# Optimization experiments

Hardware: AMD Instinct MI355X
Metric: run time of the kernel (lower is better)

Reference implementation:

```python
import jax, jax.numpy as jnp
import numpy as np

EPS = 1e-6   # torch pairwise_distance eps added inside the norm
MARGIN = 1.0


def setup_inputs() -> dict:
    key = jax.random.key(0)
    k1, k2 = jax.random.split(key)
    B, K, D = 4096, 1024, 128
    input_features = jax.random.normal(k1, (B, D), dtype=jnp.float32)
    centroids = jax.random.normal(k2, (K, D), dtype=jnp.float32)
    return {"input_features": input_features, "centroids": centroids}


def _mode_rows(idx, num_classes):
    # idx: [B, D] ints in [0, num_classes). Returns per-row mode [B].
    # torch.mode returns the smallest value among ties; jnp.argmax also
    # returns the first (smallest) index among ties, so behavior matches.
    B = idx.shape[0]
    counts = jnp.zeros((B, num_classes), jnp.int32)
    counts = counts.at[jnp.arange(B)[:, None], idx].add(1)
    return jnp.argmax(counts, axis=1)


def reference(input_features, centroids):
    B, D = input_features.shape
    K = centroids.shape[0]

    # [B, K, D] per-dimension squared differences (mse_loss with reduce=False)
    sq = (input_features[:, None, :] - centroids[None, :, :]) ** 2
    idx_min = jnp.argmin(sq, axis=1)  # [B, D] closest centroid per dim
    idx_max = jnp.argmax(sq, axis=1)  # [B, D] furthest centroid per dim

    positives = centroids[_mode_rows(idx_min, K)]  # [B, D]
    negatives = centroids[_mode_rows(idx_max, K)]  # [B, D]

    # triplet_margin_loss(margin=1, p=2, swap=True, reduction='mean');
    # torch adds eps inside the norm: ||a - b + eps||_2
    d_pos = jnp.linalg.norm(input_features - positives + EPS, axis=1)
    d_neg = jnp.linalg.norm(input_features - negatives + EPS, axis=1)
    d_swap = jnp.linalg.norm(positives - negatives + EPS, axis=1)
    d_neg = jnp.minimum(d_neg, d_swap)

    return jnp.mean(jnp.maximum(d_pos - d_neg + MARGIN, 0.0))
```

## Files before the change

### kernel.cpp

```cpp
#include <hip/hip_runtime.h>
#include <cstdint>

#define D 128
#define K 1024
#define NB 4096
#define BB 8
#define TK 64
#define FEPS 1e-6f

typedef unsigned long long u64;
typedef unsigned int u32;
typedef unsigned short u16;


__device__ __forceinline__ int vbin(float v, float vmin, float scale) {
    float fb = (v - vmin) * scale;
    fb = fminf(fmaxf(fb, 0.0f), 255.0f);
    return (int)fb;
}

__global__ __launch_bounds__(512) void prep_search_kernel(
    const float* __restrict__ cen, const float* __restrict__ x,
    u16* __restrict__ iminT, float* __restrict__ ext, float* __restrict__ out)
{
    __shared__ u64 bkeys[K];
    __shared__ u64 skeys[K];
    __shared__ float svs[K];
    __shared__ u16 shs[K];
    __shared__ u32 binstart[257];
    __shared__ u32 pfx[256];
    __shared__ u32 cursor[256];
    __shared__ float redmn[8], redmx[8];

    const int dcol = blockIdx.x;
    const int t = threadIdx.x;
    const int wave = t >> 6, lane = t & 63;
    if (dcol == 0 && t == 0) out[0] = 0.0f;

    const float v0 = cen[t * D + dcol];
    const float v1 = cen[(t + 512) * D + dcol];

    float mn = fminf(v0, v1), mx = fmaxf(v0, v1);
    #pragma unroll
    for (int s = 32; s >= 1; s >>= 1) {
        mn = fminf(mn, __shfl_xor(mn, s, 64));
        mx = fmaxf(mx, __shfl_xor(mx, s, 64));
    }
    if (lane == 0) { redmn[wave] = mn; redmx[wave] = mx; }
    if (t < 257) binstart[t] = 0u;
    if (t < 256) cursor[t] = 0u;
    __syncthreads();

    float vmin = redmn[0], vmax = redmx[0];
    #pragma unroll
    for (int w = 1; w < 8; ++w) {
        vmin = fminf(vmin, redmn[w]);
        vmax = fmaxf(vmax, redmx[w]);
    }
    const float range = vmax - vmin;
    const float scale = (range > 0.0f) ? (255.0f / range) : 0.0f;

    u32 u0 = __float_as_uint(v0), u1 = __float_as_uint(v1);
    u0 = (u0 & 0x80000000u) ? ~u0 : (u0 | 0x80000000u);
    u1 = (u1 & 0x80000000u) ? ~u1 : (u1 | 0x80000000u);
    const u64 k0 = ((u64)u0 << 32) | (u32)t;
    const u64 k1 = ((u64)u1 << 32) | (u32)(t + 512);
    const int b0v = vbin(v0, vmin, scale);
    const int b1v = vbin(v1, vmin, scale);
    atomicAdd(&binstart[b0v], 1u);
    atomicAdd(&binstart[b1v], 1u);
    __syncthreads();

    u32 myh = 0u;
    if (t < 256) { myh = binstart[t]; pfx[t] = myh; }
    __syncthreads();
    #pragma unroll
    for (int s = 1; s < 256; s <<= 1) {
        u32 add = 0u;
        if (t < 256 && t >= s) add = pfx[t - s];
        __syncthreads();
        if (t < 256) pfx[t] += add;
        __syncthreads();
    }
    if (t < 256) {
        u32 st = pfx[t] - myh;
        binstart[t] = st;
        cursor[t] = st;
    }
    if (t == 0) binstart[256] = K;
    __syncthreads();

    { u32 s0 = atomicAdd(&cursor[b0v], 1u); bkeys[s0] = k0; }
    { u32 s1 = atomicAdd(&cursor[b1v], 1u); bkeys[s1] = k1; }
    __syncthreads();

    {
        int lo = (int)binstart[b0v], hi = (int)binstart[b0v + 1];
        int r = lo;
        for (int p = lo; p < hi; ++p) r += (bkeys[p] < k0) ? 1 : 0;
        skeys[r] = k0;
    }
    {
        int lo = (int)binstart[b1v], hi = (int)binstart[b1v + 1];
        int r = lo;
        for (int p = lo; p < hi; ++p) r += (bkeys[p] < k1) ? 1 : 0;
        skeys[r] = k1;
    }
    __syncthreads();

    #pragma unroll
    for (int j = 0; j < 2; ++j) {
        int p = j * 512 + t;
        u64 kp = skeys[p];
        u32 vb = (u32)(kp >> 32);
        int p0 = p;
        while (p0 > 0 && (u32)(skeys[p0 - 1] >> 32) == vb) --p0;
        int head = (int)(skeys[p0] & 1023u);
        u32 u = (vb & 0x80000000u) ? (vb & 0x7FFFFFFFu) : ~vb;
        float v = __uint_as_float(u);
        svs[p] = v;
        shs[p] = (u16)head;
        if (p == 0)     { ext[dcol]     = v; ((int*)ext)[2 * D + dcol] = head; }
        if (p == K - 1) { ext[D + dcol] = v; ((int*)ext)[3 * D + dcol] = head; }
    }
    __syncthreads();

    #pragma unroll 1
    for (int ph = 0; ph < 2; ++ph) {
        const int b0 = ph * 2048;
        float xq[4];
        #pragma unroll
        for (int j = 0; j < 4; ++j)
            xq[j] = x[(size_t)(b0 + j * 512 + t) * D + dcol];

        #pragma unroll
        for (int r = 0; r < 4; ++r) {
            const float xv = xq[r];
            const int bx = vbin(xv, vmin, scale);
            int lo = (int)binstart[bx], hi = (int)binstart[bx + 1];
            while (lo < hi) {
                int mid = (lo + hi) >> 1;
                if (svs[mid] <= xv) lo = mid + 1; else hi = mid;
            }
            const int p1 = lo - 1, p2 = lo;
            const int c1 = p1 < 0 ? 0 : p1;
            const int c2 = p2 > K - 1 ? K - 1 : p2;
            float vv1 = svs[c1], vv2 = svs[c2];
            int h1 = shs[c1], h2 = shs[c2];
            float d1 = xv - vv1, d2 = xv - vv2;
            float s1 = d1 * d1, s2 = d2 * d2;
            if (p1 < 0) s1 = 3.4e38f;
            if (p2 > K - 1) s2 = 3.4e38f;
            int idx;
            if (s1 < s2) idx = h1;
            else if (s2 < s1) idx = h2;
            else idx = h1 < h2 ? h1 : h2;
            iminT[(size_t)dcol * NB + b0 + r * 512 + t] = (u16)idx;
        }
    }
}

__global__ __launch_bounds__(256) void mode_loss_kernel(
    const float* __restrict__ x, const float* __restrict__ cen,
    const u16* __restrict__ iminT, const float* __restrict__ ext,
    float* __restrict__ out)
{
    __shared__ float xs[BB * D];
    __shared__ u32 cntA[BB * K / 4];
    __shared__ u32 cntB[BB * K / 4];
    __shared__ int modes[2 * BB];

    const int t = threadIdx.x;
    const int b0 = blockIdx.x * BB;

    ((float4*)xs)[t] = ((const float4*)(x + (size_t)b0 * D))[t];
    {
        uint4 z = make_uint4(0u, 0u, 0u, 0u);
        uint4* a4 = (uint4*)cntA;
        uint4* b4 = (uint4*)cntB;
        #pragma unroll
        for (int j = 0; j < 2; ++j) { a4[t + 256 * j] = z; b4[t + 256 * j] = z; }
    }
    __syncthreads();

    {
        const int dd = t >> 1, half = t & 1;
        uint2 w = *(const uint2*)(iminT + (size_t)dd * NB + b0 + half * 4);
        int i0 = (int)(w.x & 0xFFFFu), i1 = (int)(w.x >> 16);
        int i2 = (int)(w.y & 0xFFFFu), i3 = (int)(w.y >> 16);
        const int rr = half * 4;
        atomicAdd(&cntA[((rr + 0) << 8) + (i0 >> 2)], 1u << ((i0 & 3) * 8));
        atomicAdd(&cntA[((rr + 1) << 8) + (i1 >> 2)], 1u << ((i1 & 3) * 8));
        atomicAdd(&cntA[((rr + 2) << 8) + (i2 >> 2)], 1u << ((i2 & 3) * 8));
        atomicAdd(&cntA[((rr + 3) << 8) + (i3 >> 2)], 1u << ((i3 & 3) * 8));
    }

    const int d = t & (D - 1);
    const int g = t >> 7;
    {
        float cminv = ext[d], cmaxv = ext[D + d];
        int cmini = ((const int*)ext)[2 * D + d];
        int cmaxi = ((const int*)ext)[3 * D + d];
        #pragma unroll
        for (int r = 0; r < 4; ++r) {
            float xv = xs[(g * 4 + r) * D + d];
            float d1 = xv - cminv;
            float d2 = xv - cmaxv;
            float s1 = d1 * d1, s2 = d2 * d2;
            int idx;
            if (s1 > s2) idx = cmini;
            else if (s2 > s1) idx = cmaxi;
            else idx = (cmini < cmaxi) ? cmini : cmaxi;
            const int rr = g * 4 + r;
            atomicAdd(&cntB[(rr << 8) + (idx >> 2)], 1u << ((idx & 3) * 8));
        }
    }
    __syncthreads();

    const int row = t >> 5;
    const int lane = t & 31;
    {
        u32 bkeyA = 0u, bkeyB = 0u;
        #pragma unroll
        for (int j = 0; j < 8; ++j) {
            const int w = j * 32 + lane;
            u32 wA = cntA[(row << 8) + w];
            u32 wB = cntB[(row << 8) + w];
            #pragma unroll
            for (int sub = 0; sub < 4; ++sub) {
                const u32 idx = (u32)(w * 4 + sub);
                u32 cA = (wA >> (sub * 8)) & 0xFFu;
                u32 cB = (wB >> (sub * 8)) & 0xFFu;
                u32 kA = (cA << 10) | (1023u - idx);
                u32 kB = (cB << 10) | (1023u - idx);
                bkeyA = kA > bkeyA ? kA : bkeyA;
                bkeyB = kB > bkeyB ? kB : bkeyB;
            }
        }
        #pragma unroll
        for (int m = 16; m >= 1; m >>= 1) {
            u32 oA = __shfl_xor(bkeyA, m);
            u32 oB = __shfl_xor(bkeyB, m);
            bkeyA = oA > bkeyA ? oA : bkeyA;
            bkeyB = oB > bkeyB ? oB : bkeyB;
        }
        if (lane == 0) {
            modes[row]      = 1023 - (int)(bkeyA & 1023u);
            modes[BB + row] = 1023 - (int)(bkeyB & 1023u);
        }
    }
    __syncthreads();

    {
        int pm = modes[row];
        int nm = modes[BB + row];
        const float* pr = cen + (size_t)pm * D;
        const float* nr = cen + (size_t)nm * D;
        float a1 = 0.f, a2 = 0.f, a3 = 0.f;
        #pragma unroll
        for (int j = 0; j < 4; ++j) {
            int dd = j * 32 + lane;
            float xv = xs[row * D + dd];
            float pv = pr[dd], nv = nr[dd];
            float e1 = xv - pv + FEPS;
            float e2 = xv - nv + FEPS;
            float e3 = pv - nv + FEPS;
            a1 += e1 * e1; a2 += e2 * e2; a3 += e3 * e3;
        }
        #pragma unroll
        for (int m = 16; m >= 1; m >>= 1) {
            a1 += __shfl_xor(a1, m);
            a2 += __shfl_xor(a2, m);
            a3 += __shfl_xor(a3, m);
        }
        if (lane == 0) {
            float dp = sqrtf(a1);
            float dneg = fminf(sqrtf(a2), sqrtf(a3));
            float term = dp - dneg + 1.0f;
            if (term > 0.f) atomicAdd(out, term * (1.0f / NB));
        }
    }
}

__global__ __launch_bounds__(256) void col_extremes_kernel(
    const float* __restrict__ cen, float* __restrict__ ws)
{
    __shared__ float mv[256]; __shared__ int mi[256];
    __shared__ float Mv[256]; __shared__ int Mi[256];
    const int dcol = blockIdx.x;
    const int t = threadIdx.x;

    float lminv = 3.4e38f; int lmini = 0;
    float lmaxv = -3.4e38f; int lmaxi = 0;
    #pragma unroll
    for (int j = 0; j < 4; ++j) {
        int k = t * 4 + j;
        float v = cen[k * D + dcol];
        if (v < lminv) { lminv = v; lmini = k; }
        if (v > lmaxv) { lmaxv = v; lmaxi = k; }
    }
    mv[t] = lminv; mi[t] = lmini; Mv[t] = lmaxv; Mi[t] = lmaxi;
    __syncthreads();
    for (int s = 128; s > 0; s >>= 1) {
        if (t < s) {
            float ov = mv[t + s]; int oi = mi[t + s];
            if (ov < mv[t] || (ov == mv[t] && oi < mi[t])) { mv[t] = ov; mi[t] = oi; }
            float Ov = Mv[t + s]; int Oi = Mi[t + s];
            if (Ov > Mv[t] || (Ov == Mv[t] && Oi < Mi[t])) { Mv[t] = Ov; Mi[t] = Oi; }
        }
        __syncthreads();
    }
    if (t == 0) {
        ws[dcol]     = mv[0];
        ws[D + dcol] = Mv[0];
        ((int*)ws)[2 * D + dcol] = mi[0];
        ((int*)ws)[3 * D + dcol] = Mi[0];
    }
}

__global__ __launch_bounds__(256) void cluster_triplet_kernel(
    const float* __restrict__ x, const float* __restrict__ cen,
    const float* __restrict__ ws, float* __restrict__ out)
{
    __shared__ float ctile[TK * D];
    __shared__ float xs[BB * D];
    __shared__ u16 imin[BB * D];
    __shared__ u16 imax[BB * D];
    __shared__ int modes[2 * BB];

    const int t = threadIdx.x;
    const int b0 = blockIdx.x * BB;

    ((float4*)xs)[t] = ((const float4*)(x + (size_t)b0 * D))[t];
    __syncthreads();

    const int d = t & (D - 1);
    const int g = t >> 7;

    float xr[4];
    #pragma unroll
    for (int r = 0; r < 4; ++r) xr[r] = xs[(g * 4 + r) * D + d];

    float best[4]; int bidx[4];
    #pragma unroll
    for (int r = 0; r < 4; ++r) { best[r] = 3.4e38f; bidx[r] = 0; }

    for (int kt = 0; kt < K / TK; ++kt) {
        __syncthreads();
        {
            const float4* src = (const float4*)(cen + (size_t)kt * TK * D);
            float4* dst = (float4*)ctile;
            #pragma unroll
            for (int j = 0; j < 8; ++j) dst[t + 256 * j] = src[t + 256 * j];
        }
        __syncthreads();
        #pragma unroll 8
        for (int kk = 0; kk < TK; ++kk) {
            float cv = ctile[kk * D + d];
            int kg = kt * TK + kk;
            #pragma unroll
            for (int r = 0; r < 4; ++r) {
                float ad = fabsf(xr[r] - cv);
                if (ad < best[r]) { best[r] = ad; bidx[r] = kg; }
            }
        }
    }

    #pragma unroll
    for (int r = 0; r < 4; ++r) imin[(g * 4 + r) * D + d] = (u16)bidx[r];

    {
        float cminv = ws[d], cmaxv = ws[D + d];
        int cmini = ((const int*)ws)[2 * D + d];
        int cmaxi = ((const int*)ws)[3 * D + d];
        #pragma unroll
        for (int r = 0; r < 4; ++r) {
            float d1 = xr[r] - cminv;
            float d2 = xr[r] - cmaxv;
            float s1 = d1 * d1, s2 = d2 * d2;
            int idx;
            if (s1 > s2) idx = cmini;
            else if (s2 > s1) idx = cmaxi;
            else idx = (cmini < cmaxi) ? cmini : cmaxi;
            imax[(g * 4 + r) * D + d] = (u16)idx;
        }
    }
    __syncthreads();

    u32* counts = (u32*)ctile;
    const int row = t >> 5;
    const int lane = t & 31;
    for (int pass = 0; pass < 2; ++pass) {
        {
            uint4* cz = (uint4*)counts;
            uint4 z = make_uint4(0u, 0u, 0u, 0u);
            #pragma unroll
            for (int j = 0; j < 8; ++j) cz[t + 256 * j] = z;
        }
        __syncthreads();
        const u16* src = (pass == 0) ? imin : imax;
        #pragma unroll
        for (int r = 0; r < 4; ++r) {
            int rr = g * 4 + r;
            atomicAdd(&counts[rr * K + (int)src[rr * D + d]], 1u);
        }
        __syncthreads();
        u32 bkey = 0u;
        for (int j = 0; j < 32; ++j) {
            int idx = j * 32 + lane;
            u32 cnt = counts[row * K + idx];
            u32 key = (cnt << 10) | (1023u - (u32)idx);
            bkey = (key > bkey) ? key : bkey;
        }
        #pragma unroll
        for (int m = 16; m >= 1; m >>= 1) {
            u32 o = __shfl_xor(bkey, m);
            bkey = (o > bkey) ? o : bkey;
        }
        if (lane == 0) modes[pass * BB + row] = 1023 - (int)(bkey & 1023u);
        __syncthreads();
    }

    {
        int pm = modes[0 * BB + row];
        int nm = modes[1 * BB + row];
        const float* pr = cen + (size_t)pm * D;
        const float* nr = cen + (size_t)nm * D;
        float a1 = 0.f, a2 = 0.f, a3 = 0.f;
        #pragma unroll
        for (int j = 0; j < 4; ++j) {
            int dd = j * 32 + lane;
            float xv = xs[row * D + dd];
            float pv = pr[dd], nv = nr[dd];
            float e1 = xv - pv + FEPS;
            float e2 = xv - nv + FEPS;
            float e3 = pv - nv + FEPS;
            a1 += e1 * e1; a2 += e2 * e2; a3 += e3 * e3;
        }
        #pragma unroll
        for (int m = 16; m >= 1; m >>= 1) {
            a1 += __shfl_xor(a1, m);
            a2 += __shfl_xor(a2, m);
            a3 += __shfl_xor(a3, m);
        }
        if (lane == 0) {
            float dp = sqrtf(a1);
            float dneg = fminf(sqrtf(a2), sqrtf(a3));
            float term = dp - dneg + 1.0f;
            if (term > 0.f) atomicAdd(out, term * (1.0f / NB));
        }
    }
}

extern "C" void kernel_launch(void* const* d_in, const int* in_sizes, int n_in,
                              void* d_out, int out_size, void* d_ws, size_t ws_size,
                              hipStream_t stream) {
    (void)in_sizes; (void)n_in; (void)out_size;
    const float* x   = (const float*)d_in[0];
    const float* cen = (const float*)d_in[1];
    float* out = (float*)d_out;

    const size_t need = (size_t)D * NB * 2
                      + (size_t)4 * D * 4;
    if (ws_size >= need) {
        u16* iminT  = (u16*)d_ws;
        float* ext  = (float*)(iminT + (size_t)D * NB);
        prep_search_kernel<<<D, 512, 0, stream>>>(cen, x, iminT, ext, out);
        mode_loss_kernel<<<NB / BB, 256, 0, stream>>>(x, cen, iminT, ext, out);
    } else {
        float* ws = (float*)d_ws;
        hipMemsetAsync(d_out, 0, sizeof(float), stream);
        col_extremes_kernel<<<D, 256, 0, stream>>>(cen, ws);
        cluster_triplet_kernel<<<NB / BB, 256, 0, stream>>>(x, cen, ws, out);
    }
}
```

Measured before the change: 95.57 us.

## Fuse search pipeline into one cooperative kernel with grid-wide syncs

Replaces the two-kernel path (per-column sort+search, then mode/loss) with a single cooperative kernel of 512 blocks that sorts each centroid column, transposes x, does binned binary-search nearest lookup spread across all blocks, then computes modes and the loss, separated by grid.sync. It also packs mode counts into byte-wide counters in shared memory to shrink LDS usage and scans both histograms together. The goal is to spread the search over more blocks than the 128 column blocks and drop a launch. In exchange it adds grid-sync overhead, extra global traffic for intermediates, and byte counters that overflow if any centroid appears more than 255 times in a row.

```diff
diff --git a/kernel.cpp b/kernel.cpp
--- a/kernel.cpp
+++ b/kernel.cpp
@@ -1,5 +1,8 @@
 #include <hip/hip_runtime.h>
+#include <hip/hip_cooperative_groups.h>
 #include <cstdint>
+
+namespace cg = cooperative_groups;
 
 #define D 128
 #define K 1024
@@ -17,6 +20,301 @@
     float fb = (v - vmin) * scale;
     fb = fminf(fmaxf(fb, 0.0f), 255.0f);
     return (int)fb;
+}
+
+struct SMemA {
+    u64 bkeys[K];
+    u64 skeys[K];
+    float svs[K];
+    u16 shs[K];
+    u32 binstart[257];
+    u32 pfx[256];
+    u32 cursor[256];
+    float red[8];
+};
+struct SMemB {
+    float svs[K];
+    u16 shs[K];
+    u32 binstart[257];
+};
+struct SMemC {
+    float xs[BB * D];
+    u32 cntA[BB * K / 4];
+    u32 cntB[BB * K / 4];
+    int modes[2 * BB];
+};
+union SMem { SMemA a; SMemB b; SMemC c; };
+
+__global__ __launch_bounds__(256, 2) void fused_kernel(
+    const float* __restrict__ cen, const float* __restrict__ x,
+    float* __restrict__ sval, u16* __restrict__ shead,
+    u32* __restrict__ binstartG, float* __restrict__ meta,
+    float* __restrict__ ext, float* __restrict__ xT,
+    u16* __restrict__ iminT, float* __restrict__ out)
+{
+    cg::grid_group grid = cg::this_grid();
+    __shared__ SMem sm;
+
+    const int bid = blockIdx.x;
+    const int t = threadIdx.x;
+
+    if (bid < D) {
+        const int dcol = bid;
+        const int wave = t >> 6, lane = t & 63;
+        if (dcol == 0 && t == 0) out[0] = 0.0f;
+
+        float v[4];
+        #pragma unroll
+        for (int j = 0; j < 4; ++j) v[j] = cen[(j * 256 + t) * D + dcol];
+
+        float mn = fminf(fminf(v[0], v[1]), fminf(v[2], v[3]));
+        float mx = fmaxf(fmaxf(v[0], v[1]), fmaxf(v[2], v[3]));
+        #pragma unroll
+        for (int s = 32; s >= 1; s >>= 1) {
+            mn = fminf(mn, __shfl_xor(mn, s, 64));
+            mx = fmaxf(mx, __shfl_xor(mx, s, 64));
+        }
+        if (lane == 0) { sm.a.red[wave] = mn; sm.a.red[4 + wave] = mx; }
+        sm.a.binstart[t] = 0u;
+        if (t == 0) sm.a.binstart[256] = 0u;
+        __syncthreads();
+
+        const float vmin = fminf(fminf(sm.a.red[0], sm.a.red[1]),
+                                 fminf(sm.a.red[2], sm.a.red[3]));
+        const float vmax = fmaxf(fmaxf(sm.a.red[4], sm.a.red[5]),
+                                 fmaxf(sm.a.red[6], sm.a.red[7]));
+        const float range = vmax - vmin;
+        const float scale = (range > 0.0f) ? (255.0f / range) : 0.0f;
+
+        u64 key[4]; int bk[4];
+        #pragma unroll
+        for (int j = 0; j < 4; ++j) {
+            u32 u = __float_as_uint(v[j]);
+            u = (u & 0x80000000u) ? ~u : (u | 0x80000000u);
+            key[j] = ((u64)u << 32) | (u32)(j * 256 + t);
+            bk[j] = vbin(v[j], vmin, scale);
+            atomicAdd(&sm.a.binstart[bk[j]], 1u);
+        }
+        __syncthreads();
+
+        u32 myh = sm.a.binstart[t];
+        sm.a.pfx[t] = myh;
+        __syncthreads();
+        #pragma unroll
+        for (int s = 1; s < 256; s <<= 1) {
+            u32 add = (t >= s) ? sm.a.pfx[t - s] : 0u;
+            __syncthreads();
+            sm.a.pfx[t] += add;
+            __syncthreads();
+        }
+        {
+            u32 st = sm.a.pfx[t] - myh;
+            sm.a.binstart[t] = st;
+            sm.a.cursor[t] = st;
+            if (t == 0) sm.a.binstart[256] = K;
+        }
+        __syncthreads();
+
+        #pragma unroll
+        for (int j = 0; j < 4; ++j) {
+            u32 s = atomicAdd(&sm.a.cursor[bk[j]], 1u);
+            sm.a.bkeys[s] = key[j];
+        }
+        __syncthreads();
+
+        #pragma unroll
+        for (int j = 0; j < 4; ++j) {
+            int lo = (int)sm.a.binstart[bk[j]], hi = (int)sm.a.binstart[bk[j] + 1];
+            int r = lo;
+            for (int p = lo; p < hi; ++p) r += (sm.a.bkeys[p] < key[j]) ? 1 : 0;
+            sm.a.skeys[r] = key[j];
+        }
+        __syncthreads();
+
+        #pragma unroll
+        for (int j = 0; j < 4; ++j) {
+            int p = j * 256 + t;
+            u64 kp = sm.a.skeys[p];
+            u32 vb = (u32)(kp >> 32);
+            int p0 = p;
+            while (p0 > 0 && (u32)(sm.a.skeys[p0 - 1] >> 32) == vb) --p0;
+            int head = (int)(sm.a.skeys[p0] & 1023u);
+            u32 u = (vb & 0x80000000u) ? (vb & 0x7FFFFFFFu) : ~vb;
+            float sv = __uint_as_float(u);
+            sval[dcol * K + p] = sv;
+            shead[dcol * K + p] = (u16)head;
+            if (p == 0)     { ext[dcol]     = sv; ((int*)ext)[2 * D + dcol] = head; }
+            if (p == K - 1) { ext[D + dcol] = sv; ((int*)ext)[3 * D + dcol] = head; }
+        }
+        binstartG[dcol * 257 + t] = sm.a.binstart[t];
+        if (t == 0) {
+            binstartG[dcol * 257 + 256] = K;
+            meta[dcol * 2 + 0] = vmin;
+            meta[dcol * 2 + 1] = scale;
+        }
+    } else if (bid < D + 256) {
+        const int tb = bid - D;
+        const int d = tb >> 1;
+        const int base = (tb & 1) * 2048;
+        #pragma unroll
+        for (int j = 0; j < 8; ++j) {
+            int b = base + j * 256 + t;
+            xT[(size_t)d * NB + b] = x[(size_t)b * D + d];
+        }
+    }
+
+    grid.sync();
+
+    {
+        const int col = bid & (D - 1);
+        const int chunk = bid >> 7;
+        ((float4*)sm.b.svs)[t] = ((const float4*)(sval + col * K))[t];
+        ((uint2*)sm.b.shs)[t]  = ((const uint2*)(shead + col * K))[t];
+        sm.b.binstart[t] = binstartG[col * 257 + t];
+        if (t == 0) sm.b.binstart[256] = binstartG[col * 257 + 256];
+        const float vmin = meta[col * 2 + 0];
+        const float scale = meta[col * 2 + 1];
+        __syncthreads();
+
+        #pragma unroll
+        for (int j = 0; j < 4; ++j) {
+            const int b = chunk * 1024 + j * 256 + t;
+            const float xv = xT[(size_t)col * NB + b];
+            const int bx = vbin(xv, vmin, scale);
+            int lo = (int)sm.b.binstart[bx], hi = (int)sm.b.binstart[bx + 1];
+            while (lo < hi) {
+                int mid = (lo + hi) >> 1;
+                if (sm.b.svs[mid] <= xv) lo = mid + 1; else hi = mid;
+            }
+            const int p1 = lo - 1, p2 = lo;
+            const int c1 = p1 < 0 ? 0 : p1;
+            const int c2 = p2 > K - 1 ? K - 1 : p2;
+            float vv1 = sm.b.svs[c1], vv2 = sm.b.svs[c2];
+            int h1 = sm.b.shs[c1], h2 = sm.b.shs[c2];
+            float d1 = xv - vv1, d2 = xv - vv2;
+            float s1 = d1 * d1, s2 = d2 * d2;
+            if (p1 < 0) s1 = 3.4e38f;
+            if (p2 > K - 1) s2 = 3.4e38f;
+            int idx;
+            if (s1 < s2) idx = h1;
+            else if (s2 < s1) idx = h2;
+            else idx = h1 < h2 ? h1 : h2;
+            iminT[(size_t)col * NB + b] = (u16)idx;
+        }
+    }
+
+    grid.sync();
+
+    {
+        const int b0 = bid * BB;
+        ((float4*)sm.c.xs)[t] = ((const float4*)(x + (size_t)b0 * D))[t];
+        {
+            uint4 z = make_uint4(0u, 0u, 0u, 0u);
+            uint4* a4 = (uint4*)sm.c.cntA;
+            uint4* b4 = (uint4*)sm.c.cntB;
+            #pragma unroll
+            for (int j = 0; j < 2; ++j) { a4[t + 256 * j] = z; b4[t + 256 * j] = z; }
+        }
+        __syncthreads();
+
+        {
+            const int dd = t >> 1, half = t & 1;
+            uint2 w = *(const uint2*)(iminT + (size_t)dd * NB + b0 + half * 4);
+            int i0 = (int)(w.x & 0xFFFFu), i1 = (int)(w.x >> 16);
+            int i2 = (int)(w.y & 0xFFFFu), i3 = (int)(w.y >> 16);
+            const int rr = half * 4;
+            atomicAdd(&sm.c.cntA[((rr + 0) << 8) + (i0 >> 2)], 1u << ((i0 & 3) * 8));
+            atomicAdd(&sm.c.cntA[((rr + 1) << 8) + (i1 >> 2)], 1u << ((i1 & 3) * 8));
+            atomicAdd(&sm.c.cntA[((rr + 2) << 8) + (i2 >> 2)], 1u << ((i2 & 3) * 8));
+            atomicAdd(&sm.c.cntA[((rr + 3) << 8) + (i3 >> 2)], 1u << ((i3 & 3) * 8));
+        }
+
+        const int d = t & (D - 1);
+        const int g = t >> 7;
+        {
+            float cminv = ext[d], cmaxv = ext[D + d];
+            int cmini = ((const int*)ext)[2 * D + d];
+            int cmaxi = ((const int*)ext)[3 * D + d];
+            #pragma unroll
+            for (int r = 0; r < 4; ++r) {
+                float xv = sm.c.xs[(g * 4 + r) * D + d];
+                float d1 = xv - cminv;
+                float d2 = xv - cmaxv;
+                float s1 = d1 * d1, s2 = d2 * d2;
+                int idx;
+                if (s1 > s2) idx = cmini;
+                else if (s2 > s1) idx = cmaxi;
+                else idx = (cmini < cmaxi) ? cmini : cmaxi;
+                const int rr = g * 4 + r;
+                atomicAdd(&sm.c.cntB[(rr << 8) + (idx >> 2)], 1u << ((idx & 3) * 8));
+            }
+        }
+        __syncthreads();
+
+        const int row = t >> 5;
+        const int lane = t & 31;
+        {
+            u32 bkeyA = 0u, bkeyB = 0u;
+            #pragma unroll
+            for (int j = 0; j < 8; ++j) {
+                const int w = j * 32 + lane;
+                u32 wA = sm.c.cntA[(row << 8) + w];
+                u32 wB = sm.c.cntB[(row << 8) + w];
+                #pragma unroll
+                for (int sub = 0; sub < 4; ++sub) {
+                    const u32 idx = (u32)(w * 4 + sub);
+                    u32 cA = (wA >> (sub * 8)) & 0xFFu;
+                    u32 cB = (wB >> (sub * 8)) & 0xFFu;
+                    u32 kA = (cA << 10) | (1023u - idx);
+                    u32 kB = (cB << 10) | (1023u - idx);
+                    bkeyA = kA > bkeyA ? kA : bkeyA;
+                    bkeyB = kB > bkeyB ? kB : bkeyB;
+                }
+            }
+            #pragma unroll
+            for (int m = 16; m >= 1; m >>= 1) {
+                u32 oA = __shfl_xor(bkeyA, m);
+                u32 oB = __shfl_xor(bkeyB, m);
+                bkeyA = oA > bkeyA ? oA : bkeyA;
+                bkeyB = oB > bkeyB ? oB : bkeyB;
+            }
+            if (lane == 0) {
+                sm.c.modes[row]      = 1023 - (int)(bkeyA & 1023u);
+                sm.c.modes[BB + row] = 1023 - (int)(bkeyB & 1023u);
+            }
+        }
+        __syncthreads();
+
+        {
+            int pm = sm.c.modes[row];
+            int nm = sm.c.modes[BB + row];
+            const float* pr = cen + (size_t)pm * D;
+            const float* nr = cen + (size_t)nm * D;
+            float a1 = 0.f, a2 = 0.f, a3 = 0.f;
+            #pragma unroll
+            for (int j = 0; j < 4; ++j) {
+                int dd = j * 32 + lane;
+                float xv = sm.c.xs[row * D + dd];
+                float pv = pr[dd], nv = nr[dd];
+                float e1 = xv - pv + FEPS;
+                float e2 = xv - nv + FEPS;
+                float e3 = pv - nv + FEPS;
+                a1 += e1 * e1; a2 += e2 * e2; a3 += e3 * e3;
+            }
+            #pragma unroll
+            for (int m = 16; m >= 1; m >>= 1) {
+                a1 += __shfl_xor(a1, m);
+                a2 += __shfl_xor(a2, m);
+                a3 += __shfl_xor(a3, m);
+            }
+            if (lane == 0) {
+                float dp = sqrtf(a1);
+                float dneg = fminf(sqrtf(a2), sqrtf(a3));
+                float term = dp - dneg + 1.0f;
+                if (term > 0.f) atomicAdd(out, term * (1.0f / NB));
+            }
+        }
+    }
 }
 
 __global__ __launch_bounds__(512) void prep_search_kernel(
@@ -282,176 +580,6 @@
     }
 }
 
-__global__ __launch_bounds__(256) void col_extremes_kernel(
-    const float* __restrict__ cen, float* __restrict__ ws)
-{
-    __shared__ float mv[256]; __shared__ int mi[256];
-    __shared__ float Mv[256]; __shared__ int Mi[256];
-    const int dcol = blockIdx.x;
-    const int t = threadIdx.x;
-
-    float lminv = 3.4e38f; int lmini = 0;
-    float lmaxv = -3.4e38f; int lmaxi = 0;
-    #pragma unroll
-    for (int j = 0; j < 4; ++j) {
-        int k = t * 4 + j;
-        float v = cen[k * D + dcol];
-        if (v < lminv) { lminv = v; lmini = k; }
-        if (v > lmaxv) { lmaxv = v; lmaxi = k; }
-    }
-    mv[t] = lminv; mi[t] = lmini; Mv[t] = lmaxv; Mi[t] = lmaxi;
-    __syncthreads();
-    for (int s = 128; s > 0; s >>= 1) {
-        if (t < s) {
-            float ov = mv[t + s]; int oi = mi[t + s];
-            if (ov < mv[t] || (ov == mv[t] && oi < mi[t])) { mv[t] = ov; mi[t] = oi; }
-            float Ov = Mv[t + s]; int Oi = Mi[t + s];
-            if (Ov > Mv[t] || (Ov == Mv[t] && Oi < Mi[t])) { Mv[t] = Ov; Mi[t] = Oi; }
-        }
-        __syncthreads();
-    }
-    if (t == 0) {
-        ws[dcol]     = mv[0];
-        ws[D + dcol] = Mv[0];
-        ((int*)ws)[2 * D + dcol] = mi[0];
-        ((int*)ws)[3 * D + dcol] = Mi[0];
-    }
-}
-
-__global__ __launch_bounds__(256) void cluster_triplet_kernel(
-    const float* __restrict__ x, const float* __restrict__ cen,
-    const float* __restrict__ ws, float* __restrict__ out)
-{
-    __shared__ float ctile[TK * D];
-    __shared__ float xs[BB * D];
-    __shared__ u16 imin[BB * D];
-    __shared__ u16 imax[BB * D];
-    __shared__ int modes[2 * BB];
-
-    const int t = threadIdx.x;
-    const int b0 = blockIdx.x * BB;
-
-    ((float4*)xs)[t] = ((const float4*)(x + (size_t)b0 * D))[t];
-    __syncthreads();
-
-    const int d = t & (D - 1);
-    const int g = t >> 7;
-
-    float xr[4];
-    #pragma unroll
-    for (int r = 0; r < 4; ++r) xr[r] = xs[(g * 4 + r) * D + d];
-
-    float best[4]; int bidx[4];
-    #pragma unroll
-    for (int r = 0; r < 4; ++r) { best[r] = 3.4e38f; bidx[r] = 0; }
-
-    for (int kt = 0; kt < K / TK; ++kt) {
-        __syncthreads();
-        {
-            const float4* src = (const float4*)(cen + (size_t)kt * TK * D);
-            float4* dst = (float4*)ctile;
-            #pragma unroll
-            for (int j = 0; j < 8; ++j) dst[t + 256 * j] = src[t + 256 * j];
-        }
-        __syncthreads();
-        #pragma unroll 8
-        for (int kk = 0; kk < TK; ++kk) {
-            float cv = ctile[kk * D + d];
-            int kg = kt * TK + kk;
-            #pragma unroll
-            for (int r = 0; r < 4; ++r) {
-                float ad = fabsf(xr[r] - cv);
-                if (ad < best[r]) { best[r] = ad; bidx[r] = kg; }
-            }
-        }
-    }
-
-    #pragma unroll
-    for (int r = 0; r < 4; ++r) imin[(g * 4 + r) * D + d] = (u16)bidx[r];
-
-    {
-        float cminv = ws[d], cmaxv = ws[D + d];
-        int cmini = ((const int*)ws)[2 * D + d];
-        int cmaxi = ((const int*)ws)[3 * D + d];
-        #pragma unroll
-        for (int r = 0; r < 4; ++r) {
-            float d1 = xr[r] - cminv;
-            float d2 = xr[r] - cmaxv;
-            float s1 = d1 * d1, s2 = d2 * d2;
-            int idx;
-            if (s1 > s2) idx = cmini;
-            else if (s2 > s1) idx = cmaxi;
-            else idx = (cmini < cmaxi) ? cmini : cmaxi;
-            imax[(g * 4 + r) * D + d] = (u16)idx;
-        }
-    }
-    __syncthreads();
-
-    u32* counts = (u32*)ctile;
-    const int row = t >> 5;
-    const int lane = t & 31;
-    for (int pass = 0; pass < 2; ++pass) {
-        {
-            uint4* cz = (uint4*)counts;
-            uint4 z = make_uint4(0u, 0u, 0u, 0u);
-            #pragma unroll
-            for (int j = 0; j < 8; ++j) cz[t + 256 * j] = z;
-        }
-        __syncthreads();
-        const u16* src = (pass == 0) ? imin : imax;
-        #pragma unroll
-        for (int r = 0; r < 4; ++r) {
-            int rr = g * 4 + r;
-            atomicAdd(&counts[rr * K + (int)src[rr * D + d]], 1u);
-        }
-        __syncthreads();
-        u32 bkey = 0u;
-        for (int j = 0; j < 32; ++j) {
-            int idx = j * 32 + lane;
-            u32 cnt = counts[row * K + idx];
-            u32 key = (cnt << 10) | (1023u - (u32)idx);
-            bkey = (key > bkey) ? key : bkey;
-        }
-        #pragma unroll
-        for (int m = 16; m >= 1; m >>= 1) {
-            u32 o = __shfl_xor(bkey, m);
-            bkey = (o > bkey) ? o : bkey;
-        }
-        if (lane == 0) modes[pass * BB + row] = 1023 - (int)(bkey & 1023u);
-        __syncthreads();
-    }
-
-    {
-        int pm = modes[0 * BB + row];
-        int nm = modes[1 * BB + row];
-        const float* pr = cen + (size_t)pm * D;
-        const float* nr = cen + (size_t)nm * D;
-        float a1 = 0.f, a2 = 0.f, a3 = 0.f;
-        #pragma unroll
-        for (int j = 0; j < 4; ++j) {
-            int dd = j * 32 + lane;
-            float xv = xs[row * D + dd];
-            float pv = pr[dd], nv = nr[dd];
-            float e1 = xv - pv + FEPS;
-            float e2 = xv - nv + FEPS;
-            float e3 = pv - nv + FEPS;
-            a1 += e1 * e1; a2 += e2 * e2; a3 += e3 * e3;
-        }
-        #pragma unroll
-        for (int m = 16; m >= 1; m >>= 1) {
-            a1 += __shfl_xor(a1, m);
-            a2 += __shfl_xor(a2, m);
-            a3 += __shfl_xor(a3, m);
-        }
-        if (lane == 0) {
-            float dp = sqrtf(a1);
-            float dneg = fminf(sqrtf(a2), sqrtf(a3));
-            float term = dp - dneg + 1.0f;
-            if (term > 0.f) atomicAdd(out, term * (1.0f / NB));
-        }
-    }
-}
-
 extern "C" void kernel_launch(void* const* d_in, const int* in_sizes, int n_in,
                               void* d_out, int out_size, void* d_ws, size_t ws_size,
                               hipStream_t stream) {
@@ -460,17 +588,32 @@
     const float* cen = (const float*)d_in[1];
     float* out = (float*)d_out;
 
-    const size_t need = (size_t)D * NB * 2
-                      + (size_t)4 * D * 4;
+    char* ws = (char*)d_ws;
+    float* sval      = (float*)(ws + 0);
+    float* xT        = (float*)(ws + 524288);
+    float* ext       = (float*)(ws + 2621440);
+    float* meta      = (float*)(ws + 2623488);
+    u32*   binstartG = (u32*)  (ws + 2624512);
+    u16*   shead     = (u16*)  (ws + 2756096);
+    u16*   iminT     = (u16*)  (ws + 3018240);
+    const size_t need = 3018240 + (size_t)D * NB * 2;
+
     if (ws_size >= need) {
-        u16* iminT  = (u16*)d_ws;
-        float* ext  = (float*)(iminT + (size_t)D * NB);
-        prep_search_kernel<<<D, 512, 0, stream>>>(cen, x, iminT, ext, out);
-        mode_loss_kernel<<<NB / BB, 256, 0, stream>>>(x, cen, iminT, ext, out);
+        const float* cen_a = cen; const float* x_a = x; float* out_a = out;
+        void* args[] = { (void*)&cen_a, (void*)&x_a, (void*)&sval, (void*)&shead,
+                         (void*)&binstartG, (void*)&meta, (void*)&ext, (void*)&xT,
+                         (void*)&iminT, (void*)&out_a };
+        hipError_t e = hipLaunchCooperativeKernel(
+            (const void*)fused_kernel, dim3(512), dim3(256), args, 0, stream);
+        if (e != hipSuccess) {
+            (void)hipGetLastError();
+            prep_search_kernel<<<D, 512, 0, stream>>>(cen, x, iminT, ext, out);
+            mode_loss_kernel<<<NB / BB, 256, 0, stream>>>(x, cen, iminT, ext, out);
+        }
     } else {
-        float* ws = (float*)d_ws;
-        hipMemsetAsync(d_out, 0, sizeof(float), stream);
-        col_extremes_kernel<<<D, 256, 0, stream>>>(cen, ws);
-        cluster_triplet_kernel<<<NB / BB, 256, 0, stream>>>(x, cen, ws, out);
+        u16* iminT2 = (u16*)d_ws;
+        float* ext2 = (float*)(iminT2 + (size_t)D * NB);
+        prep_search_kernel<<<D, 512, 0, stream>>>(cen, x, iminT2, ext2, out);
+        mode_loss_kernel<<<NB / BB, 256, 0, stream>>>(x, cen, iminT2, ext2, out);
     }
 }
```

Result: slower. 229.8 us (+140.5%).

## Split prep/search into separate kernels to parallelize per-column search across more blocks

Applied to the files above, without the earlier changes.

The fused per-column sort+search kernel is split in two. A prep kernel sorts the centroid column and writes the sorted values, heads, bin starts and min/scale to workspace. A new search kernel launches 8 blocks per column (1024 blocks in total) so the binary search over all 4096 rows runs on many more CUs. The old 128-block kernel serialized the search inside each block. The change adds an extra launch and a workspace round trip, and it removes the small-workspace fallback path.

```diff
diff --git a/kernel.cpp b/kernel.cpp
--- a/kernel.cpp
+++ b/kernel.cpp
@@ -5,7 +5,6 @@
 #define K 1024
 #define NB 4096
 #define BB 8
-#define TK 64
 #define FEPS 1e-6f
 
 typedef unsigned long long u64;
@@ -19,14 +18,13 @@
     return (int)fb;
 }
 
-__global__ __launch_bounds__(512) void prep_search_kernel(
-    const float* __restrict__ cen, const float* __restrict__ x,
-    u16* __restrict__ iminT, float* __restrict__ ext, float* __restrict__ out)
+__global__ __launch_bounds__(512) void prep_kernel(
+    const float* __restrict__ cen, float* __restrict__ sval,
+    u16* __restrict__ shead, u32* __restrict__ binstartG,
+    float* __restrict__ meta, float* __restrict__ ext, float* __restrict__ out)
 {
     __shared__ u64 bkeys[K];
     __shared__ u64 skeys[K];
-    __shared__ float svs[K];
-    __shared__ u16 shs[K];
     __shared__ u32 binstart[257];
     __shared__ u32 pfx[256];
     __shared__ u32 cursor[256];
@@ -118,45 +116,68 @@
         int head = (int)(skeys[p0] & 1023u);
         u32 u = (vb & 0x80000000u) ? (vb & 0x7FFFFFFFu) : ~vb;
         float v = __uint_as_float(u);
-        svs[p] = v;
-        shs[p] = (u16)head;
+        sval[dcol * K + p] = v;
+        shead[dcol * K + p] = (u16)head;
         if (p == 0)     { ext[dcol]     = v; ((int*)ext)[2 * D + dcol] = head; }
         if (p == K - 1) { ext[D + dcol] = v; ((int*)ext)[3 * D + dcol] = head; }
     }
-    __syncthreads();
-
-    #pragma unroll 1
-    for (int ph = 0; ph < 2; ++ph) {
-        const int b0 = ph * 2048;
-        float xq[4];
-        #pragma unroll
-        for (int j = 0; j < 4; ++j)
-            xq[j] = x[(size_t)(b0 + j * 512 + t) * D + dcol];
-
-        #pragma unroll
-        for (int r = 0; r < 4; ++r) {
-            const float xv = xq[r];
-            const int bx = vbin(xv, vmin, scale);
-            int lo = (int)binstart[bx], hi = (int)binstart[bx + 1];
-            while (lo < hi) {
-                int mid = (lo + hi) >> 1;
-                if (svs[mid] <= xv) lo = mid + 1; else hi = mid;
-            }
-            const int p1 = lo - 1, p2 = lo;
-            const int c1 = p1 < 0 ? 0 : p1;
-            const int c2 = p2 > K - 1 ? K - 1 : p2;
-            float vv1 = svs[c1], vv2 = svs[c2];
-            int h1 = shs[c1], h2 = shs[c2];
-            float d1 = xv - vv1, d2 = xv - vv2;
-            float s1 = d1 * d1, s2 = d2 * d2;
-            if (p1 < 0) s1 = 3.4e38f;
-            if (p2 > K - 1) s2 = 3.4e38f;
-            int idx;
-            if (s1 < s2) idx = h1;
-            else if (s2 < s1) idx = h2;
-            else idx = h1 < h2 ? h1 : h2;
-            iminT[(size_t)dcol * NB + b0 + r * 512 + t] = (u16)idx;
-        }
+    if (t < 257) binstartG[dcol * 257 + t] = binstart[t];
+    if (t == 0) {
+        meta[dcol * 2 + 0] = vmin;
+        meta[dcol * 2 + 1] = scale;
+    }
+}
+
+__global__ __launch_bounds__(256) void search_kernel(
+    const float* __restrict__ x, const float* __restrict__ sval,
+    const u16* __restrict__ shead, const u32* __restrict__ binstartG,
+    const float* __restrict__ meta, u16* __restrict__ iminT)
+{
+    __shared__ float svs[K];
+    __shared__ u16 shs[K];
+    __shared__ u32 binstart[257];
+
+    const int col = blockIdx.x & (D - 1);
+    const int chunk = blockIdx.x >> 7;
+    const int t = threadIdx.x;
+
+    ((float4*)svs)[t] = ((const float4*)(sval + col * K))[t];
+    ((uint2*)shs)[t]  = ((const uint2*)(shead + col * K))[t];
+    binstart[t] = binstartG[col * 257 + t];
+    if (t == 0) binstart[256] = binstartG[col * 257 + 256];
+    const float vmin = meta[col * 2 + 0];
+    const float scale = meta[col * 2 + 1];
+    __syncthreads();
+
+    const int b0 = chunk * 512;
+    float xq[2];
+    #pragma unroll
+    for (int j = 0; j < 2; ++j)
+        xq[j] = x[(size_t)(b0 + j * 256 + t) * D + col];
+
+    #pragma unroll
+    for (int j = 0; j < 2; ++j) {
+        const float xv = xq[j];
+        const int bx = vbin(xv, vmin, scale);
+        int lo = (int)binstart[bx], hi = (int)binstart[bx + 1];
+        while (lo < hi) {
+            int mid = (lo + hi) >> 1;
+            if (svs[mid] <= xv) lo = mid + 1; else hi = mid;
+        }
+        const int p1 = lo - 1, p2 = lo;
+        const int c1 = p1 < 0 ? 0 : p1;
+        const int c2 = p2 > K - 1 ? K - 1 : p2;
+        float vv1 = svs[c1], vv2 = svs[c2];
+        int h1 = shs[c1], h2 = shs[c2];
+        float d1 = xv - vv1, d2 = xv - vv2;
+        float s1 = d1 * d1, s2 = d2 * d2;
+        if (p1 < 0) s1 = 3.4e38f;
+        if (p2 > K - 1) s2 = 3.4e38f;
+        int idx;
+        if (s1 < s2) idx = h1;
+        else if (s2 < s1) idx = h2;
+        else idx = h1 < h2 ? h1 : h2;
+        iminT[(size_t)col * NB + b0 + j * 256 + t] = (u16)idx;
     }
 }
 
@@ -282,195 +303,23 @@
     }
 }
 
-__global__ __launch_bounds__(256) void col_extremes_kernel(
-    const float* __restrict__ cen, float* __restrict__ ws)
-{
-    __shared__ float mv[256]; __shared__ int mi[256];
-    __shared__ float Mv[256]; __shared__ int Mi[256];
-    const int dcol = blockIdx.x;
-    const int t = threadIdx.x;
-
-    float lminv = 3.4e38f; int lmini = 0;
-    float lmaxv = -3.4e38f; int lmaxi = 0;
-    #pragma unroll
-    for (int j = 0; j < 4; ++j) {
-        int k = t * 4 + j;
-        float v = cen[k * D + dcol];
-        if (v < lminv) { lminv = v; lmini = k; }
-        if (v > lmaxv) { lmaxv = v; lmaxi = k; }
-    }
-    mv[t] = lminv; mi[t] = lmini; Mv[t] = lmaxv; Mi[t] = lmaxi;
-    __syncthreads();
-    for (int s = 128; s > 0; s >>= 1) {
-        if (t < s) {
-            float ov = mv[t + s]; int oi = mi[t + s];
-            if (ov < mv[t] || (ov == mv[t] && oi < mi[t])) { mv[t] = ov; mi[t] = oi; }
-            float Ov = Mv[t + s]; int Oi = Mi[t + s];
-            if (Ov > Mv[t] || (Ov == Mv[t] && Oi < Mi[t])) { Mv[t] = Ov; Mi[t] = Oi; }
-        }
-        __syncthreads();
-    }
-    if (t == 0) {
-        ws[dcol]     = mv[0];
-        ws[D + dcol] = Mv[0];
-        ((int*)ws)[2 * D + dcol] = mi[0];
-        ((int*)ws)[3 * D + dcol] = Mi[0];
-    }
-}
-
-__global__ __launch_bounds__(256) void cluster_triplet_kernel(
-    const float* __restrict__ x, const float* __restrict__ cen,
-    const float* __restrict__ ws, float* __restrict__ out)
-{
-    __shared__ float ctile[TK * D];
-    __shared__ float xs[BB * D];
-    __shared__ u16 imin[BB * D];
-    __shared__ u16 imax[BB * D];
-    __shared__ int modes[2 * BB];
-
-    const int t = threadIdx.x;
-    const int b0 = blockIdx.x * BB;
-
-    ((float4*)xs)[t] = ((const float4*)(x + (size_t)b0 * D))[t];
-    __syncthreads();
-
-    const int d = t & (D - 1);
-    const int g = t >> 7;
-
-    float xr[4];
-    #pragma unroll
-    for (int r = 0; r < 4; ++r) xr[r] = xs[(g * 4 + r) * D + d];
-
-    float best[4]; int bidx[4];
-    #pragma unroll
-    for (int r = 0; r < 4; ++r) { best[r] = 3.4e38f; bidx[r] = 0; }
-
-    for (int kt = 0; kt < K / TK; ++kt) {
-        __syncthreads();
-        {
-            const float4* src = (const float4*)(cen + (size_t)kt * TK * D);
-            float4* dst = (float4*)ctile;
-            #pragma unroll
-            for (int j = 0; j < 8; ++j) dst[t + 256 * j] = src[t + 256 * j];
-        }
-        __syncthreads();
-        #pragma unroll 8
-        for (int kk = 0; kk < TK; ++kk) {
-            float cv = ctile[kk * D + d];
-            int kg = kt * TK + kk;
-            #pragma unroll
-            for (int r = 0; r < 4; ++r) {
-                float ad = fabsf(xr[r] - cv);
-                if (ad < best[r]) { best[r] = ad; bidx[r] = kg; }
-            }
-        }
-    }
-
-    #pragma unroll
-    for (int r = 0; r < 4; ++r) imin[(g * 4 + r) * D + d] = (u16)bidx[r];
-
-    {
-        float cminv = ws[d], cmaxv = ws[D + d];
-        int cmini = ((const int*)ws)[2 * D + d];
-        int cmaxi = ((const int*)ws)[3 * D + d];
-        #pragma unroll
-        for (int r = 0; r < 4; ++r) {
-            float d1 = xr[r] - cminv;
-            float d2 = xr[r] - cmaxv;
-            float s1 = d1 * d1, s2 = d2 * d2;
-            int idx;
-            if (s1 > s2) idx = cmini;
-            else if (s2 > s1) idx = cmaxi;
-            else idx = (cmini < cmaxi) ? cmini : cmaxi;
-            imax[(g * 4 + r) * D + d] = (u16)idx;
-        }
-    }
-    __syncthreads();
-
-    u32* counts = (u32*)ctile;
-    const int row = t >> 5;
-    const int lane = t & 31;
-    for (int pass = 0; pass < 2; ++pass) {
-        {
-            uint4* cz = (uint4*)counts;
-            uint4 z = make_uint4(0u, 0u, 0u, 0u);
-            #pragma unroll
-            for (int j = 0; j < 8; ++j) cz[t + 256 * j] = z;
-        }
-        __syncthreads();
-        const u16* src = (pass == 0) ? imin : imax;
-        #pragma unroll
-        for (int r = 0; r < 4; ++r) {
-            int rr = g * 4 + r;
-            atomicAdd(&counts[rr * K + (int)src[rr * D + d]], 1u);
-        }
-        __syncthreads();
-        u32 bkey = 0u;
-        for (int j = 0; j < 32; ++j) {
-            int idx = j * 32 + lane;
-            u32 cnt = counts[row * K + idx];
-            u32 key = (cnt << 10) | (1023u - (u32)idx);
-            bkey = (key > bkey) ? key : bkey;
-        }
-        #pragma unroll
-        for (int m = 16; m >= 1; m >>= 1) {
-            u32 o = __shfl_xor(bkey, m);
-            bkey = (o > bkey) ? o : bkey;
-        }
-        if (lane == 0) modes[pass * BB + row] = 1023 - (int)(bkey & 1023u);
-        __syncthreads();
-    }
-
-    {
-        int pm = modes[0 * BB + row];
-        int nm = modes[1 * BB + row];
-        const float* pr = cen + (size_t)pm * D;
-        const float* nr = cen + (size_t)nm * D;
-        float a1 = 0.f, a2 = 0.f, a3 = 0.f;
-        #pragma unroll
-        for (int j = 0; j < 4; ++j) {
-            int dd = j * 32 + lane;
-            float xv = xs[row * D + dd];
-            float pv = pr[dd], nv = nr[dd];
-            float e1 = xv - pv + FEPS;
-            float e2 = xv - nv + FEPS;
-            float e3 = pv - nv + FEPS;
-            a1 += e1 * e1; a2 += e2 * e2; a3 += e3 * e3;
-        }
-        #pragma unroll
-        for (int m = 16; m >= 1; m >>= 1) {
-            a1 += __shfl_xor(a1, m);
-            a2 += __shfl_xor(a2, m);
-            a3 += __shfl_xor(a3, m);
-        }
-        if (lane == 0) {
-            float dp = sqrtf(a1);
-            float dneg = fminf(sqrtf(a2), sqrtf(a3));
-            float term = dp - dneg + 1.0f;
-            if (term > 0.f) atomicAdd(out, term * (1.0f / NB));
-        }
-    }
-}
-
 extern "C" void kernel_launch(void* const* d_in, const int* in_sizes, int n_in,
                               void* d_out, int out_size, void* d_ws, size_t ws_size,
                               hipStream_t stream) {
-    (void)in_sizes; (void)n_in; (void)out_size;
+    (void)in_sizes; (void)n_in; (void)out_size; (void)ws_size;
     const float* x   = (const float*)d_in[0];
     const float* cen = (const float*)d_in[1];
     float* out = (float*)d_out;
 
-    const size_t need = (size_t)D * NB * 2
-                      + (size_t)4 * D * 4;
-    if (ws_size >= need) {
-        u16* iminT  = (u16*)d_ws;
-        float* ext  = (float*)(iminT + (size_t)D * NB);
-        prep_search_kernel<<<D, 512, 0, stream>>>(cen, x, iminT, ext, out);
-        mode_loss_kernel<<<NB / BB, 256, 0, stream>>>(x, cen, iminT, ext, out);
-    } else {
-        float* ws = (float*)d_ws;
-        hipMemsetAsync(d_out, 0, sizeof(float), stream);
-        col_extremes_kernel<<<D, 256, 0, stream>>>(cen, ws);
-        cluster_triplet_kernel<<<NB / BB, 256, 0, stream>>>(x, cen, ws, out);
-    }
-}
+    char* ws = (char*)d_ws;
+    float* sval      = (float*)(ws + 0);
+    u16*   shead     = (u16*)  (ws + 524288);
+    u32*   binstartG = (u32*)  (ws + 786432);
+    float* meta      = (float*)(ws + 918016);
+    float* ext       = (float*)(ws + 919040);
+    u16*   iminT     = (u16*)  (ws + 921088);
+
+    prep_kernel<<<D, 512, 0, stream>>>(cen, sval, shead, binstartG, meta, ext, out);
+    search_kernel<<<D * 8, 256, 0, stream>>>(x, sval, shead, binstartG, meta, iminT);
+    mode_loss_kernel<<<NB / BB, 256, 0, stream>>>(x, cen, iminT, ext, out);
+}
```

After: 95.52 us. About the same (-0.1%).
